# Kernel tuning notes

Hardware: AMD Instinct MI355X
Metric: run time of the kernel (lower is better)

## Reference

```python
import jax, jax.numpy as jnp
import numpy as np

EMBED = 1024
HEADS = 16
HEAD_DIM = EMBED // HEADS


def setup_inputs() -> dict:
    key = jax.random.key(0)
    ks = jax.random.split(key, 6)
    B, S, E = 2, 2048, EMBED
    x = jax.random.normal(ks[0], (B, S, E), dtype=jnp.float32)
    # torch nn.Linear stores weight as [out, in]; scale ~ 1/sqrt(E) like default init
    sc = 1.0 / np.sqrt(E)
    Wq = jax.random.normal(ks[1], (E, E), dtype=jnp.float32) * sc
    Wk = jax.random.normal(ks[2], (E, E), dtype=jnp.float32) * sc
    Wv = jax.random.normal(ks[3], (E, E), dtype=jnp.float32) * sc
    Wo = jax.random.normal(ks[4], (E, E), dtype=jnp.float32) * sc
    bo = jnp.zeros((E,), dtype=jnp.float32)
    # causal mask, broadcastable [1,1,S,S]; mask==0 positions get -inf
    mask = jnp.tril(jnp.ones((S, S), dtype=jnp.int32))[None, None]
    return {"x": x, "mask": mask, "Wq": Wq, "Wk": Wk, "Wv": Wv, "Wo": Wo, "bo": bo}


def reference(x, mask, Wq, Wk, Wv, Wo, bo):
    B, S, E = x.shape
    # Linear(x) = x @ W.T (torch convention, no bias)
    Q = (x @ Wq.T).reshape(B, S, HEADS, HEAD_DIM).transpose(0, 2, 1, 3)  # [B,H,S,D]
    K = (x @ Wk.T).reshape(B, S, HEADS, HEAD_DIM).transpose(0, 2, 1, 3)
    V = (x @ Wv.T).reshape(B, S, HEADS, HEAD_DIM).transpose(0, 2, 1, 3)
    scale = 1.0 / jnp.sqrt(jnp.float32(HEAD_DIM))
    scores = jnp.einsum("bhqd,bhkd->bhqk", Q, K) * scale  # [B,H,S,S]
    scores = jnp.where(mask == 0, -jnp.inf, scores)
    attn = jax.nn.softmax(scores, axis=-1)
    out = jnp.einsum("bhqk,bhkd->bhqd", attn, V)  # [B,H,S,D]
    out = out.transpose(0, 2, 1, 3).reshape(B, S, E)
    return out @ Wo.T + bo
```

## Files before the change

kernel.cpp:

```cpp
#include <hip/hip_runtime.h>
#include <hip/hip_bf16.h>

typedef unsigned short u16;
typedef unsigned int u32;

#define B_ 2
#define S_ 2048
#define E_ 1024
#define H_ 16
#define D_ 64

typedef __bf16 bf16_8 __attribute__((ext_vector_type(8)));
typedef __bf16 bf16_4 __attribute__((ext_vector_type(4)));
typedef float f32_4 __attribute__((ext_vector_type(4)));

typedef const __attribute__((address_space(1))) void* gptr_t;
typedef __attribute__((address_space(3))) void* sptr_t;

__device__ __forceinline__ void gload_lds16(const void* g, void* l) {
  __builtin_amdgcn_global_load_lds((gptr_t)g, (sptr_t)l, 16, 0, 0);
}

__device__ __forceinline__ u16 f2bf(float f) {
  union { float f; u32 u; } v; v.f = f;
  u32 u = v.u;
  u32 r = (u + 0x7FFFu + ((u >> 16) & 1u)) >> 16;
  return (u16)r;
}

#define MFMA16 __builtin_amdgcn_mfma_f32_16x16x32_bf16

__global__ __launch_bounds__(256) void cvt_all(
    const float* __restrict__ x,
    const float* __restrict__ wq, const float* __restrict__ wk,
    const float* __restrict__ wv, const float* __restrict__ wo,
    u16* __restrict__ dst)
{
  const int XB = (B_ * S_ * E_) / 1024;
  const int WB = (E_ * E_) / 1024;
  int blk = blockIdx.x;
  const float* src;
  size_t dbase;
  if (blk < XB)           { src = x;  dbase = 0;                         }
  else if (blk < XB+WB)   { src = wq; dbase = (size_t)B_*S_*E_;          blk -= XB; }
  else if (blk < XB+2*WB) { src = wk; dbase = (size_t)B_*S_*E_ + E_*E_;  blk -= XB+WB; }
  else if (blk < XB+3*WB) { src = wv; dbase = (size_t)B_*S_*E_ + 2*(size_t)E_*E_; blk -= XB+2*WB; }
  else                    { src = wo; dbase = (size_t)B_*S_*E_ + 3*(size_t)E_*E_; blk -= XB+3*WB; }
  size_t i = ((size_t)blk * 256 + threadIdx.x) * 4;
  float4 v = *(const float4*)(src + i);
  ushort4 o;
  o.x = f2bf(v.x); o.y = f2bf(v.y); o.z = f2bf(v.z); o.w = f2bf(v.w);
  *(ushort4*)(dst + dbase + i) = o;
}

#define TST 136
__global__ __launch_bounds__(256) void qkv_gemm(
    const u16* __restrict__ x,
    const u16* __restrict__ wq, const u16* __restrict__ wk, const u16* __restrict__ wv,
    u16* __restrict__ q_ws, u16* __restrict__ k_ws, u16* __restrict__ v_ws)
{
  const int K = E_;
  __shared__ __attribute__((aligned(16))) u16 SM[16384];
  u16* As = SM;
  u16* Bs = SM + 8192;
  u16* LB = SM;

  int tid = threadIdx.x;
  int wave = tid >> 6, lane = tid & 63;
  int quad = lane >> 4, fcol = lane & 15;
  int row0 = blockIdx.x * 128;
  int nb = blockIdx.y;
  int which = nb >> 3;
  const u16* W = (which == 0) ? wq : ((which == 1) ? wk : wv);
  int col0 = (nb & 7) * 128;
  int wm = wave >> 1, wn = wave & 1;
  int swzb = fcol & 7;

  f32_4 acc[4][4];
#pragma unroll
  for (int i = 0; i < 4; i++)
#pragma unroll
    for (int j = 0; j < 4; j++) acc[i][j] = f32_4{0.f, 0.f, 0.f, 0.f};

  for (int k0 = 0; k0 < K; k0 += 64) {
#pragma unroll
    for (int i = 0; i < 4; i++) {
      int c = i * 256 + tid;
      int r = c >> 3;
      int kcd = (c & 7) ^ (r & 7);
      gload_lds16(x + (size_t)(row0 + r) * K + k0 + kcd * 8, As + (size_t)c * 8);
      gload_lds16(W + (size_t)(col0 + r) * K + k0 + kcd * 8, Bs + (size_t)c * 8);
    }
    __syncthreads();
#pragma unroll
    for (int ks2 = 0; ks2 < 2; ks2++) {
      bf16_8 a[4], b[4];
#pragma unroll
      for (int mt = 0; mt < 4; mt++) {
        int rm = wm * 64 + mt * 16 + fcol;
        a[mt] = *(const bf16_8*)(As + rm * 64 + (((ks2 * 4 + quad) ^ swzb) << 3));
      }
#pragma unroll
      for (int nt = 0; nt < 4; nt++) {
        int rn = wn * 64 + nt * 16 + fcol;
        b[nt] = *(const bf16_8*)(Bs + rn * 64 + (((ks2 * 4 + quad) ^ swzb) << 3));
      }
#pragma unroll
      for (int mt = 0; mt < 4; mt++)
#pragma unroll
        for (int nt = 0; nt < 4; nt++)
          acc[mt][nt] = MFMA16(a[mt], b[nt], acc[mt][nt], 0, 0, 0);
    }
    __syncthreads();
  }

  if (which != 2) {
    u16* dst = (which == 0) ? q_ws : k_ws;
#pragma unroll
    for (int p = 0; p < 2; p++) {
      if (wm == p) {
#pragma unroll
        for (int mt = 0; mt < 4; mt++)
#pragma unroll
          for (int nt = 0; nt < 4; nt++)
#pragma unroll
            for (int r = 0; r < 4; r++)
              LB[(mt * 16 + quad * 4 + r) * TST + wn * 64 + nt * 16 + fcol] =
                  f2bf(acc[mt][nt][r]);
      }
      __syncthreads();
#pragma unroll
      for (int i = 0; i < 4; i++) {
        int r_loc = i * 16 + (tid >> 4);
        int c8 = (tid & 15) * 8;
        int hh = (col0 + c8) >> 6, d = c8 & (D_ - 1);
        int grow = row0 + p * 64 + r_loc;
        int b = grow >> 11, s = grow & (S_ - 1);
        *(bf16_8*)(dst + (((size_t)b * H_ + hh) * S_ + s) * D_ + d) =
            *(const bf16_8*)(LB + r_loc * TST + c8);
      }
      __syncthreads();
    }
  } else {
    int b = row0 >> 11, s0 = row0 & (S_ - 1);
#pragma unroll
    for (int p = 0; p < 2; p++) {
      if (wn == p) {
#pragma unroll
        for (int mt = 0; mt < 4; mt++)
#pragma unroll
          for (int nt = 0; nt < 4; nt++)
#pragma unroll
            for (int r = 0; r < 4; r++)
              LB[(nt * 16 + fcol) * TST + wm * 64 + mt * 16 + quad * 4 + r] =
                  f2bf(acc[mt][nt][r]);
      }
      __syncthreads();
      {
        int fl = tid >> 2, tq = tid & 3;
        int F = col0 + p * 64 + fl;
        int h = F >> 6, d = F & (D_ - 1);
        u16* vp = v_ws + (((size_t)b * H_ + h) * D_ + d) * S_ + s0 + tq * 32;
#pragma unroll
        for (int i = 0; i < 4; i++)
          *(bf16_8*)(vp + i * 8) = *(const bf16_8*)(LB + fl * TST + tq * 32 + i * 8);
      }
      __syncthreads();
    }
  }
}

__global__ __launch_bounds__(256, 3) void attn_kernel(
    const u16* __restrict__ Qg_, const u16* __restrict__ Kg_,
    const u16* __restrict__ Vg_, u16* __restrict__ Og_)
{
  __shared__ __attribute__((aligned(16))) u16 KV[16384];
  __shared__ __attribute__((aligned(16))) u16 Ps[8192];

  int tid = threadIdx.x, wave = tid >> 6, lane = tid & 63;
  int quad = lane >> 4, fcol = lane & 15;
  int blk = blockIdx.x;
  int bh = blk & 31;
  int qi = blk >> 5;
  int b = bh >> 4, h = bh & (H_ - 1);
  int nt_tiles = 2 * qi + 2;

  const u16* Qg = Qg_ + (size_t)bh * S_ * D_;
  const u16* Kg = Kg_ + (size_t)bh * S_ * D_;
  const u16* Vg = Vg_ + (size_t)bh * D_ * S_;

  int qbw = qi * 128 + wave * 32;
  int sw = fcol & 7;

  bf16_8 aq[2][2];
#pragma unroll
  for (int f = 0; f < 2; f++)
#pragma unroll
    for (int ks2 = 0; ks2 < 2; ks2++)
      aq[f][ks2] = *(const bf16_8*)(Qg + (size_t)(qbw + f * 16 + fcol) * D_ + ks2 * 32 + quad * 8);

  auto stage = [&](int j, int buf) {
    u16* Kb = KV + buf * 8192;
#pragma unroll
    for (int i = 0; i < 2; i++) {
      int c = (i << 8) + tid;
      int r = c >> 3;
      int kcd = (c & 7) ^ (r & 7);
      gload_lds16(Kg + (size_t)(j * 64 + r) * D_ + kcd * 8, Kb + c * 8);
      gload_lds16(Vg + (size_t)r * S_ + j * 64 + kcd * 8, Kb + 4096 + c * 8);
    }
  };

  stage(0, 0);
  asm volatile("s_waitcnt vmcnt(0)" ::: "memory");
  __syncthreads();

  const __bf16 one = (__bf16)1.0f;
  const bf16_8 vone = {one, one, one, one, one, one, one, one};

  f32_4 accO[2][4];
  f32_4 accL[2];
#pragma unroll
  for (int f = 0; f < 2; f++) {
    accL[f] = f32_4{0.f, 0.f, 0.f, 0.f};
#pragma unroll
    for (int n = 0; n < 4; n++) accO[f][n] = f32_4{0.f, 0.f, 0.f, 0.f};
  }

  u16* Pw = Ps + wave * 2048;

  for (int j = 0; j < nt_tiles; j++) {
    const u16* Kb = KV + (j & 1) * 8192;
    const u16* Vb = Kb + 4096;
    if (j + 1 < nt_tiles) stage(j + 1, (j & 1) ^ 1);

    bf16_8 bk[2][4];
#pragma unroll
    for (int ks2 = 0; ks2 < 2; ks2++)
#pragma unroll
      for (int n = 0; n < 4; n++)
        bk[ks2][n] = *(const bf16_8*)(Kb + (n * 16 + fcol) * 64 + (((ks2 * 4 + quad) ^ sw) << 3));

    f32_4 sc[2][4];
#pragma unroll
    for (int f = 0; f < 2; f++)
#pragma unroll
      for (int n = 0; n < 4; n++) sc[f][n] = f32_4{0.f, 0.f, 0.f, 0.f};
    __builtin_amdgcn_s_setprio(1);
#pragma unroll
    for (int f = 0; f < 2; f++)
#pragma unroll
      for (int ks2 = 0; ks2 < 2; ks2++)
#pragma unroll
        for (int n = 0; n < 4; n++)
          sc[f][n] = MFMA16(aq[f][ks2], bk[ks2][n], sc[f][n], 0, 0, 0);
    __builtin_amdgcn_s_setprio(0);

    float p[2][4][4];
#pragma unroll
    for (int f = 0; f < 2; f++) {
#pragma unroll
      for (int n = 0; n < 4; n++)
#pragma unroll
        for (int r = 0; r < 4; r++)
          p[f][n][r] = __expf(fmaf(sc[f][n][r], 0.125f, -12.0f));
      int frmin = qbw + f * 16;
      if (64 * j + 63 > frmin) {
        int qrow0 = frmin + quad * 4;
#pragma unroll
        for (int n = 0; n < 4; n++) {
          int kv = j * 64 + n * 16 + fcol;
#pragma unroll
          for (int r = 0; r < 4; r++)
            if (kv > qrow0 + r) p[f][n][r] = 0.f;
        }
      }
    }

#pragma unroll
    for (int f = 0; f < 2; f++)
#pragma unroll
      for (int n = 0; n < 4; n++) {
        int ch = n * 2 + (fcol >> 3);
#pragma unroll
        for (int r = 0; r < 4; r++) {
          int row = f * 16 + quad * 4 + r;
          Pw[row * 64 + ((ch ^ (row & 7)) << 3) + (fcol & 7)] = f2bf(p[f][n][r]);
        }
      }

    bf16_8 bv[2][4];
#pragma unroll
    for (int ks2 = 0; ks2 < 2; ks2++)
#pragma unroll
      for (int n = 0; n < 4; n++)
        bv[ks2][n] = *(const bf16_8*)(Vb + (n * 16 + fcol) * 64 + (((ks2 * 4 + quad) ^ sw) << 3));

    __builtin_amdgcn_s_setprio(1);
#pragma unroll
    for (int f = 0; f < 2; f++)
#pragma unroll
      for (int ks2 = 0; ks2 < 2; ks2++) {
        bf16_8 ap = *(const bf16_8*)(Pw + (f * 16 + fcol) * 64 + (((ks2 * 4 + quad) ^ sw) << 3));
        accL[f] = MFMA16(ap, vone, accL[f], 0, 0, 0);
#pragma unroll
        for (int n = 0; n < 4; n++)
          accO[f][n] = MFMA16(ap, bv[ks2][n], accO[f][n], 0, 0, 0);
      }
    __builtin_amdgcn_s_setprio(0);

    if (j + 1 < nt_tiles) __syncthreads();
  }

#pragma unroll
  for (int f = 0; f < 2; f++)
#pragma unroll
    for (int r = 0; r < 4; r++) {
      float inv = 1.0f / accL[f][r];
      int qrow = qbw + f * 16 + quad * 4 + r;
#pragma unroll
      for (int n = 0; n < 4; n++) {
        int d = n * 16 + fcol;
        Og_[((size_t)b * S_ + qrow) * E_ + h * D_ + d] = f2bf(accO[f][n][r] * inv);
      }
    }
}

__global__ __launch_bounds__(256) void out_gemm(
    const u16* __restrict__ A, const u16* __restrict__ W,
    const float* __restrict__ bias, float* __restrict__ out)
{
  const int K = E_;
  __shared__ __attribute__((aligned(16))) u16 As[128 * 64];
  __shared__ __attribute__((aligned(16))) u16 Bs[64 * 64];

  int tid = threadIdx.x;
  int wave = tid >> 6, lane = tid & 63;
  int quad = lane >> 4, fcol = lane & 15;
  int row0 = blockIdx.x * 128;
  int col0 = blockIdx.y * 64;
  int swzb = fcol & 7;

  f32_4 acc[2][4];
#pragma unroll
  for (int i = 0; i < 2; i++)
#pragma unroll
    for (int j = 0; j < 4; j++) acc[i][j] = f32_4{0.f, 0.f, 0.f, 0.f};

  for (int k0 = 0; k0 < K; k0 += 64) {
#pragma unroll
    for (int i = 0; i < 4; i++) {
      int c = i * 256 + tid;
      int r = c >> 3;
      int kcd = (c & 7) ^ (r & 7);
      gload_lds16(A + (size_t)(row0 + r) * K + k0 + kcd * 8, As + (size_t)c * 8);
    }
#pragma unroll
    for (int i = 0; i < 2; i++) {
      int c = i * 256 + tid;
      int r = c >> 3;
      int kcd = (c & 7) ^ (r & 7);
      gload_lds16(W + (size_t)(col0 + r) * K + k0 + kcd * 8, Bs + (size_t)c * 8);
    }
    __syncthreads();
#pragma unroll
    for (int ks2 = 0; ks2 < 2; ks2++) {
      bf16_8 a[2], b[4];
#pragma unroll
      for (int mt = 0; mt < 2; mt++) {
        int rm = wave * 32 + mt * 16 + fcol;
        a[mt] = *(const bf16_8*)(As + rm * 64 + (((ks2 * 4 + quad) ^ swzb) << 3));
      }
#pragma unroll
      for (int nt = 0; nt < 4; nt++) {
        int rn = nt * 16 + fcol;
        b[nt] = *(const bf16_8*)(Bs + rn * 64 + (((ks2 * 4 + quad) ^ swzb) << 3));
      }
#pragma unroll
      for (int mt = 0; mt < 2; mt++)
#pragma unroll
        for (int nt = 0; nt < 4; nt++)
          acc[mt][nt] = MFMA16(a[mt], b[nt], acc[mt][nt], 0, 0, 0);
    }
    __syncthreads();
  }

#pragma unroll
  for (int mt = 0; mt < 2; mt++)
#pragma unroll
    for (int nt = 0; nt < 4; nt++) {
      int gcol = col0 + nt * 16 + fcol;
      float bv = bias[gcol];
#pragma unroll
      for (int r = 0; r < 4; r++) {
        int grow = row0 + wave * 32 + mt * 16 + quad * 4 + r;
        out[(size_t)grow * E_ + gcol] = acc[mt][nt][r] + bv;
      }
    }
}

extern "C" void kernel_launch(void* const* d_in, const int* in_sizes, int n_in,
                              void* d_out, int out_size, void* d_ws, size_t ws_size,
                              hipStream_t stream) {
  const float* x  = (const float*)d_in[0];
  const float* wq = (const float*)d_in[2];
  const float* wk = (const float*)d_in[3];
  const float* wv = (const float*)d_in[4];
  const float* wo = (const float*)d_in[5];
  const float* bo = (const float*)d_in[6];
  float* out = (float*)d_out;

  const size_t sz  = (size_t)B_ * S_ * E_;
  const size_t wsz = (size_t)E_ * E_;
  if (ws_size < (5 * sz + 4 * wsz) * sizeof(u16)) return;

  u16* x_bf  = (u16*)d_ws;
  u16* wq_bf = x_bf + sz;
  u16* wk_bf = wq_bf + wsz;
  u16* wv_bf = wk_bf + wsz;
  u16* wo_bf = wv_bf + wsz;
  u16* q_ws  = wo_bf + wsz;
  u16* k_ws  = q_ws + sz;
  u16* v_ws  = k_ws + sz;
  u16* o_ws  = v_ws + sz;

  cvt_all<<<(int)((sz + 4 * wsz) / 1024), 256, 0, stream>>>(x, wq, wk, wv, wo, x_bf);
  qkv_gemm<<<dim3(32, 24), 256, 0, stream>>>(x_bf, wq_bf, wk_bf, wv_bf, q_ws, k_ws, v_ws);
  attn_kernel<<<dim3(512), 256, 0, stream>>>(q_ws, k_ws, v_ws, o_ws);
  out_gemm<<<dim3(32, 16), 256, 0, stream>>>(o_ws, wo_bf, bo, out);
}
```

Before: 211.4 us.

## Split attention into single-wave blocks with direct register K/V loads

The attention kernel moves from 256-thread blocks handling 128 query rows to 64-thread single-wave blocks handling 32 rows, launched as 2048 blocks. The longest causal blocks are ordered first to balance load. The shared-memory K/V double buffer and block barriers are gone: each wave loads K/V fragments straight from global memory into registers and prefetches the next 32-key tile, using LDS only for a small swizzled P buffer. This removes barrier and LDS staging costs and improves scheduling granularity, but K/V reuse across waves is lost, so global/L2 traffic rises and loads become narrow strided reads.

```diff
diff --git a/kernel.cpp b/kernel.cpp
--- a/kernel.cpp
+++ b/kernel.cpp
@@ -170,27 +170,26 @@
   }
 }
 
-__global__ __launch_bounds__(256, 3) void attn_kernel(
+__global__ __launch_bounds__(64, 4) void attn_kernel(
     const u16* __restrict__ Qg_, const u16* __restrict__ Kg_,
     const u16* __restrict__ Vg_, u16* __restrict__ Og_)
 {
-  __shared__ __attribute__((aligned(16))) u16 KV[16384];
-  __shared__ __attribute__((aligned(16))) u16 Ps[8192];
-
-  int tid = threadIdx.x, wave = tid >> 6, lane = tid & 63;
+  __shared__ __attribute__((aligned(16))) u16 Ps[1024];
+
+  int lane = threadIdx.x;
   int quad = lane >> 4, fcol = lane & 15;
-  int blk = blockIdx.x;
-  int bh = blk & 31;
-  int qi = blk >> 5;
+  int u = blockIdx.x;
+  int bh = u & 31;
+  int g = u >> 5;
+  int qi = (g < 32) ? (63 - g) : (g - 32);
   int b = bh >> 4, h = bh & (H_ - 1);
-  int nt_tiles = 2 * qi + 2;
+  int nt = qi + 1;
 
   const u16* Qg = Qg_ + (size_t)bh * S_ * D_;
   const u16* Kg = Kg_ + (size_t)bh * S_ * D_;
   const u16* Vg = Vg_ + (size_t)bh * D_ * S_;
 
-  int qbw = qi * 128 + wave * 32;
-  int sw = fcol & 7;
+  int qbw = qi * 32;
 
   bf16_8 aq[2][2];
 #pragma unroll
@@ -199,22 +198,6 @@
     for (int ks2 = 0; ks2 < 2; ks2++)
       aq[f][ks2] = *(const bf16_8*)(Qg + (size_t)(qbw + f * 16 + fcol) * D_ + ks2 * 32 + quad * 8);
 
-  auto stage = [&](int j, int buf) {
-    u16* Kb = KV + buf * 8192;
-#pragma unroll
-    for (int i = 0; i < 2; i++) {
-      int c = (i << 8) + tid;
-      int r = c >> 3;
-      int kcd = (c & 7) ^ (r & 7);
-      gload_lds16(Kg + (size_t)(j * 64 + r) * D_ + kcd * 8, Kb + c * 8);
-      gload_lds16(Vg + (size_t)r * S_ + j * 64 + kcd * 8, Kb + 4096 + c * 8);
-    }
-  };
-
-  stage(0, 0);
-  asm volatile("s_waitcnt vmcnt(0)" ::: "memory");
-  __syncthreads();
-
   const __bf16 one = (__bf16)1.0f;
   const bf16_8 vone = {one, one, one, one, one, one, one, one};
 
@@ -224,52 +207,61 @@
   for (int f = 0; f < 2; f++) {
     accL[f] = f32_4{0.f, 0.f, 0.f, 0.f};
 #pragma unroll
-    for (int n = 0; n < 4; n++) accO[f][n] = f32_4{0.f, 0.f, 0.f, 0.f};
+    for (int dt = 0; dt < 4; dt++) accO[f][dt] = f32_4{0.f, 0.f, 0.f, 0.f};
   }
 
-  u16* Pw = Ps + wave * 2048;
-
-  for (int j = 0; j < nt_tiles; j++) {
-    const u16* Kb = KV + (j & 1) * 8192;
-    const u16* Vb = Kb + 4096;
-    if (j + 1 < nt_tiles) stage(j + 1, (j & 1) ^ 1);
-
-    bf16_8 bk[2][4];
-#pragma unroll
-    for (int ks2 = 0; ks2 < 2; ks2++)
-#pragma unroll
-      for (int n = 0; n < 4; n++)
-        bk[ks2][n] = *(const bf16_8*)(Kb + (n * 16 + fcol) * 64 + (((ks2 * 4 + quad) ^ sw) << 3));
-
-    f32_4 sc[2][4];
+  bf16_8 bk[2][2], bv[4];
+#pragma unroll
+  for (int ks2 = 0; ks2 < 2; ks2++)
+#pragma unroll
+    for (int n = 0; n < 2; n++)
+      bk[ks2][n] = *(const bf16_8*)(Kg + (size_t)(n * 16 + fcol) * D_ + ks2 * 32 + quad * 8);
+#pragma unroll
+  for (int dt = 0; dt < 4; dt++)
+    bv[dt] = *(const bf16_8*)(Vg + (size_t)(dt * 16 + fcol) * S_ + quad * 8);
+
+  int wr_hi = fcol >> 3;
+  int rd_x = quad ^ (fcol & 3) ^ ((fcol >> 2) & 3);
+
+  for (int j = 0; j < nt; j++) {
+    f32_4 sc[2][2];
 #pragma unroll
     for (int f = 0; f < 2; f++)
 #pragma unroll
-      for (int n = 0; n < 4; n++) sc[f][n] = f32_4{0.f, 0.f, 0.f, 0.f};
+      for (int n = 0; n < 2; n++) sc[f][n] = f32_4{0.f, 0.f, 0.f, 0.f};
     __builtin_amdgcn_s_setprio(1);
 #pragma unroll
     for (int f = 0; f < 2; f++)
 #pragma unroll
       for (int ks2 = 0; ks2 < 2; ks2++)
 #pragma unroll
-        for (int n = 0; n < 4; n++)
+        for (int n = 0; n < 2; n++)
           sc[f][n] = MFMA16(aq[f][ks2], bk[ks2][n], sc[f][n], 0, 0, 0);
     __builtin_amdgcn_s_setprio(0);
 
-    float p[2][4][4];
-#pragma unroll
-    for (int f = 0; f < 2; f++) {
-#pragma unroll
-      for (int n = 0; n < 4; n++)
+    if (j + 1 < nt) {
+#pragma unroll
+      for (int ks2 = 0; ks2 < 2; ks2++)
+#pragma unroll
+        for (int n = 0; n < 2; n++)
+          bk[ks2][n] = *(const bf16_8*)(Kg + (size_t)((j + 1) * 32 + n * 16 + fcol) * D_ + ks2 * 32 + quad * 8);
+    }
+
+    float p[2][2][4];
+#pragma unroll
+    for (int f = 0; f < 2; f++)
+#pragma unroll
+      for (int n = 0; n < 2; n++)
 #pragma unroll
         for (int r = 0; r < 4; r++)
           p[f][n][r] = __expf(fmaf(sc[f][n][r], 0.125f, -12.0f));
-      int frmin = qbw + f * 16;
-      if (64 * j + 63 > frmin) {
-        int qrow0 = frmin + quad * 4;
-#pragma unroll
-        for (int n = 0; n < 4; n++) {
-          int kv = j * 64 + n * 16 + fcol;
+    if (j == qi) {
+#pragma unroll
+      for (int f = 0; f < 2; f++) {
+        int qrow0 = qbw + f * 16 + quad * 4;
+#pragma unroll
+        for (int n = 0; n < 2; n++) {
+          int kv = j * 32 + n * 16 + fcol;
 #pragma unroll
           for (int r = 0; r < 4; r++)
             if (kv > qrow0 + r) p[f][n][r] = 0.f;
@@ -280,36 +272,34 @@
 #pragma unroll
     for (int f = 0; f < 2; f++)
 #pragma unroll
-      for (int n = 0; n < 4; n++) {
-        int ch = n * 2 + (fcol >> 3);
+      for (int n = 0; n < 2; n++)
 #pragma unroll
         for (int r = 0; r < 4; r++) {
           int row = f * 16 + quad * 4 + r;
-          Pw[row * 64 + ((ch ^ (row & 7)) << 3) + (fcol & 7)] = f2bf(p[f][n][r]);
+          int ch = (2 * n + wr_hi) ^ r ^ quad;
+          Ps[row * 32 + ch * 8 + (fcol & 7)] = f2bf(p[f][n][r]);
         }
-      }
-
-    bf16_8 bv[2][4];
-#pragma unroll
-    for (int ks2 = 0; ks2 < 2; ks2++)
-#pragma unroll
-      for (int n = 0; n < 4; n++)
-        bv[ks2][n] = *(const bf16_8*)(Vb + (n * 16 + fcol) * 64 + (((ks2 * 4 + quad) ^ sw) << 3));
+
+    bf16_8 ap[2];
+#pragma unroll
+    for (int f = 0; f < 2; f++)
+      ap[f] = *(const bf16_8*)(Ps + (f * 16 + fcol) * 32 + rd_x * 8);
 
     __builtin_amdgcn_s_setprio(1);
 #pragma unroll
-    for (int f = 0; f < 2; f++)
-#pragma unroll
-      for (int ks2 = 0; ks2 < 2; ks2++) {
-        bf16_8 ap = *(const bf16_8*)(Pw + (f * 16 + fcol) * 64 + (((ks2 * 4 + quad) ^ sw) << 3));
-        accL[f] = MFMA16(ap, vone, accL[f], 0, 0, 0);
-#pragma unroll
-        for (int n = 0; n < 4; n++)
-          accO[f][n] = MFMA16(ap, bv[ks2][n], accO[f][n], 0, 0, 0);
-      }
+    for (int f = 0; f < 2; f++) {
+      accL[f] = MFMA16(ap[f], vone, accL[f], 0, 0, 0);
+#pragma unroll
+      for (int dt = 0; dt < 4; dt++)
+        accO[f][dt] = MFMA16(ap[f], bv[dt], accO[f][dt], 0, 0, 0);
+    }
     __builtin_amdgcn_s_setprio(0);
 
-    if (j + 1 < nt_tiles) __syncthreads();
+    if (j + 1 < nt) {
+#pragma unroll
+      for (int dt = 0; dt < 4; dt++)
+        bv[dt] = *(const bf16_8*)(Vg + (size_t)(dt * 16 + fcol) * S_ + (j + 1) * 32 + quad * 8);
+    }
   }
 
 #pragma unroll
@@ -319,9 +309,9 @@
       float inv = 1.0f / accL[f][r];
       int qrow = qbw + f * 16 + quad * 4 + r;
 #pragma unroll
-      for (int n = 0; n < 4; n++) {
-        int d = n * 16 + fcol;
-        Og_[((size_t)b * S_ + qrow) * E_ + h * D_ + d] = f2bf(accO[f][n][r] * inv);
+      for (int dt = 0; dt < 4; dt++) {
+        int d = dt * 16 + fcol;
+        Og_[((size_t)b * S_ + qrow) * E_ + h * D_ + d] = f2bf(accO[f][dt][r] * inv);
       }
     }
 }
@@ -426,6 +416,6 @@
 
   cvt_all<<<(int)((sz + 4 * wsz) / 1024), 256, 0, stream>>>(x, wq, wk, wv, wo, x_bf);
   qkv_gemm<<<dim3(32, 24), 256, 0, stream>>>(x_bf, wq_bf, wk_bf, wv_bf, q_ws, k_ws, v_ws);
-  attn_kernel<<<dim3(512), 256, 0, stream>>>(q_ws, k_ws, v_ws, o_ws);
+  attn_kernel<<<dim3(2048), 64, 0, stream>>>(q_ws, k_ws, v_ws, o_ws);
   out_gemm<<<dim3(32, 16), 256, 0, stream>>>(o_ws, wo_bf, bo, out);
 }
```

Measured after the change: 222.1 us. 1.05x slower.
